# Kernel optimization log

Measured on AMD Instinct MI355X. Metric: run time of the kernel, lower is better.

## Reference

```python
import jax, jax.numpy as jnp
import numpy as np

DIM = 1024
NUM_HEADS = 16
HEAD_DIM = DIM // NUM_HEADS


def setup_inputs() -> dict:
    key = jax.random.key(0)
    k_x, k_q, k_k, k_v, k_o = jax.random.split(key, 5)
    B, L = 2, 2048
    scale = 1.0 / np.sqrt(DIM)
    x_bld = jax.random.normal(k_x, (B, L, DIM), dtype=jnp.float32)
    # LinearGeneral kernels: (in_features, num_heads, head_dim) for q/k/v,
    # (num_heads, head_dim, out_features) for out. Init ~ lecun_normal-ish scale.
    Wq = jax.random.normal(k_q, (DIM, NUM_HEADS, HEAD_DIM), dtype=jnp.float32) * scale
    Wk = jax.random.normal(k_k, (DIM, NUM_HEADS, HEAD_DIM), dtype=jnp.float32) * scale
    Wv = jax.random.normal(k_v, (DIM, NUM_HEADS, HEAD_DIM), dtype=jnp.float32) * scale
    Wo = jax.random.normal(k_o, (NUM_HEADS, HEAD_DIM, DIM), dtype=jnp.float32) * scale
    return {"x_bld": x_bld, "Wq": Wq, "Wk": Wk, "Wv": Wv, "Wo": Wo}


def reference(x_bld, Wq, Wk, Wv, Wo) -> jnp.ndarray:
    # Projections: [B,L,D] x [D,H,hd] -> [B,L,H,hd]
    q_blhd = jnp.einsum('bld,dhk->blhk', x_bld, Wq)
    k_blhd = jnp.einsum('bld,dhk->blhk', x_bld, Wk)
    v_blhd = jnp.einsum('bld,dhk->blhk', x_bld, Wv)
    # Scores: [B,H,L,L]
    attn_bhll = jnp.einsum('bqhd,bkhd->bhqk', q_blhd, k_blhd)
    attn_bhll = attn_bhll / jnp.sqrt(jnp.asarray(HEAD_DIM, dtype=attn_bhll.dtype))
    L = x_bld.shape[1]
    qi = jnp.arange(L)[:, None]
    ki = jnp.arange(L)[None, :]
    mask_ll = ki <= qi  # causal, no window
    neg_inf = jnp.finfo(attn_bhll.dtype).min
    attn_bhll = jnp.where(mask_ll[None, None, :, :], attn_bhll, neg_inf)
    attn_bhll = jax.nn.softmax(attn_bhll, axis=-1)
    y_blhd = jnp.einsum('bhqk,bkhd->bqhd', attn_bhll, v_blhd)
    # Output projection: contract (H, hd) -> D
    return jnp.einsum('blhk,hkd->bld', y_blhd, Wo)
```

## Files before the change

### kernel.cpp

```cpp
#include <hip/hip_runtime.h>
#include <hip/hip_bf16.h>

typedef __hip_bfloat16 bf16;
typedef __attribute__((ext_vector_type(8))) short short8;
typedef __attribute__((ext_vector_type(4))) float f32x4;

__device__ __forceinline__ float bfbits2f(unsigned short u) {
    return __uint_as_float(((unsigned int)u) << 16);
}
__device__ __forceinline__ unsigned short f2bfbits(float f) {
    union { float f; unsigned int u; } x;
    x.f = f;
    unsigned int r = x.u + 0x7FFFu + ((x.u >> 16) & 1u);
    return (unsigned short)(r >> 16);
}
__device__ __forceinline__ unsigned int pack_bf16x2(float lo, float hi) {
    unsigned int u0 = __float_as_uint(lo) + 0x8000u;
    unsigned int u1 = __float_as_uint(hi) + 0x8000u;
    return __builtin_amdgcn_perm(u1, u0, 0x07060302u);
}
__device__ __forceinline__ void async_copy16(const void* g, void* l) {
    __builtin_amdgcn_global_load_lds(
        (const __attribute__((address_space(1))) void*)g,
        (__attribute__((address_space(3))) void*)l, 16, 0, 0);
}

__global__ __launch_bounds__(256) void detect_dtype(
    const unsigned int* __restrict__ p0, const unsigned int* __restrict__ p1,
    const unsigned int* __restrict__ p2, const unsigned int* __restrict__ p3,
    const unsigned int* __restrict__ p4, int* __restrict__ flags) {
    const unsigned int* ps[5] = {p0, p1, p2, p3, p4};
    const unsigned int* p = ps[blockIdx.x];
    const int tid = threadIdx.x;
    int cnt = 0;
    for (int i = tid; i < 4096; i += 256) {
        unsigned int e = (p[i] >> 7) & 0xFFu;
        cnt += (e >= 90u && e <= 150u) ? 1 : 0;
    }
    __shared__ int r[256];
    r[tid] = cnt;
    __syncthreads();
    for (int off = 128; off; off >>= 1) {
        if (tid < off) r[tid] += r[tid + off];
        __syncthreads();
    }
    if (tid == 0) flags[blockIdx.x] = (r[0] > 2048) ? 1 : 0;
}

__global__ __launch_bounds__(256) void conv_x(const void* __restrict__ X,
                                              short* __restrict__ xb,
                                              const int* __restrict__ flags) {
    const bool isBf = flags[0] != 0;
    const int i = (blockIdx.x * 256 + threadIdx.x) * 8;
    if (isBf) {
        *(short8*)&xb[i] = *(const short8*)((const short*)X + i);
    } else {
        const float* xf = (const float*)X + i;
        float4 a = *(const float4*)xf;
        float4 b = *(const float4*)(xf + 4);
        short8 o;
        o[0] = (short)f2bfbits(a.x); o[1] = (short)f2bfbits(a.y);
        o[2] = (short)f2bfbits(a.z); o[3] = (short)f2bfbits(a.w);
        o[4] = (short)f2bfbits(b.x); o[5] = (short)f2bfbits(b.y);
        o[6] = (short)f2bfbits(b.z); o[7] = (short)f2bfbits(b.w);
        *(short8*)&xb[i] = o;
    }
}

__global__ __launch_bounds__(256) void conv_wT(
    const void* __restrict__ W1, const void* __restrict__ W2,
    const void* __restrict__ W3, const void* __restrict__ W4,
    short* __restrict__ O1, short* __restrict__ O2,
    short* __restrict__ O3, short* __restrict__ O4,
    const int* __restrict__ flags) {
    const void* Ws[4] = {W1, W2, W3, W4};
    short* Os[4] = {O1, O2, O3, O4};
    const int wsel = blockIdx.z;
    const bool isBf = flags[wsel + 1] != 0;
    const float scale = (wsel == 0) ? 0.125f : 1.0f;
    const void* W = Ws[wsel];
    short* O = Os[wsel];

    __shared__ float t[32][33];
    const int tx = threadIdx.x & 31;
    const int ty = threadIdx.x >> 5;
    const int gx = blockIdx.x * 32 + tx;
#pragma unroll
    for (int i = 0; i < 4; i++) {
        const int gy = blockIdx.y * 32 + ty + i * 8;
        float v = isBf ? bfbits2f(((const unsigned short*)W)[(size_t)gy * 1024 + gx])
                       : ((const float*)W)[(size_t)gy * 1024 + gx];
        t[ty + i * 8][tx] = v * scale;
    }
    __syncthreads();
#pragma unroll
    for (int i = 0; i < 4; i++) {
        const int orow = blockIdx.x * 32 + ty + i * 8;
        const int ocol = blockIdx.y * 32 + tx;
        O[(size_t)orow * 1024 + ocol] = (short)f2bfbits(t[tx][ty + i * 8]);
    }
}

__global__ __launch_bounds__(256) void transpose_v(const short* __restrict__ qkv,
                                                   short* __restrict__ VtG) {
    __shared__ short t[32][33];
    const int tx = threadIdx.x & 31, ty = threadIdx.x >> 5;
    const int b = blockIdx.z >> 4, h = blockIdx.z & 15;
    const int l0 = blockIdx.x * 32, d0 = blockIdx.y * 32;
#pragma unroll
    for (int i = 0; i < 4; i++) {
        const int l = l0 + ty + i * 8;
        t[ty + i * 8][tx] =
            qkv[(size_t)(b * 2048 + l) * 3072 + 2048 + h * 64 + d0 + tx];
    }
    __syncthreads();
    const int ptx = 2 * (tx & 15) + (tx >> 4);
#pragma unroll
    for (int i = 0; i < 4; i++) {
        const int d = d0 + ty + i * 8;
        VtG[((size_t)(b * 16 + h) * 64 + d) * 2048 + l0 + ptx] = t[tx][ty + i * 8];
    }
}

template <int BN>
__global__ __launch_bounds__(256) void gemm_async(const short* __restrict__ A,
                                                  const short* __restrict__ Bt,
                                                  void* __restrict__ C,
                                                  const int* __restrict__ flags,
                                                  int outIdx, int M, int N, int K) {
    __shared__ short As[2][128 * 32];
    __shared__ short Bs[2][BN * 32];
    constexpr int NI = BN / 32;

    const int tid = threadIdx.x;
    const int lane = tid & 63;
    const int wv = __builtin_amdgcn_readfirstlane(tid >> 6);
    const int quad = lane >> 4, l16 = lane & 15;
    const int wr = wv >> 1, wc = wv & 1;
    const int m0 = blockIdx.y * 128, n0 = blockIdx.x * BN;

    const int gr = lane >> 2;
    const int gc = (lane & 3) * 8;

    const f32x4 zero = {0.f, 0.f, 0.f, 0.f};
    f32x4 acc[4][NI];
#pragma unroll
    for (int mi = 0; mi < 4; mi++)
#pragma unroll
        for (int ni = 0; ni < NI; ni++) acc[mi][ni] = zero;

    const short* aptr[2];
    const short* bptr[BN / 64];
#pragma unroll
    for (int t = 0; t < 2; t++)
        aptr[t] = A + (size_t)(m0 + t * 64 + wv * 16 + gr) * K + gc;
#pragma unroll
    for (int t = 0; t < BN / 64; t++)
        bptr[t] = Bt + (size_t)(n0 + t * 64 + wv * 16 + gr) * K + gc;

#pragma unroll
    for (int t = 0; t < 2; t++) async_copy16(aptr[t], &As[0][(t * 64 + wv * 16) * 32]);
#pragma unroll
    for (int t = 0; t < BN / 64; t++) async_copy16(bptr[t], &Bs[0][(t * 64 + wv * 16) * 32]);

    for (int k0 = 0; k0 < K; k0 += 32) {
        const int cur = (k0 >> 5) & 1;
        __syncthreads();
        if (k0 + 32 < K) {
            const int nxt = cur ^ 1;
#pragma unroll
            for (int t = 0; t < 2; t++)
                async_copy16(aptr[t] + k0 + 32, &As[nxt][(t * 64 + wv * 16) * 32]);
#pragma unroll
            for (int t = 0; t < BN / 64; t++)
                async_copy16(bptr[t] + k0 + 32, &Bs[nxt][(t * 64 + wv * 16) * 32]);
        }

        short8 af[4], bfv[NI];
#pragma unroll
        for (int mi = 0; mi < 4; mi++)
            af[mi] = *(const short8*)&As[cur][(wr * 64 + mi * 16 + l16) * 32 + quad * 8];
#pragma unroll
        for (int ni = 0; ni < NI; ni++)
            bfv[ni] = *(const short8*)&Bs[cur][(wc * (BN / 2) + ni * 16 + l16) * 32 + quad * 8];
#pragma unroll
        for (int mi = 0; mi < 4; mi++)
#pragma unroll
            for (int ni = 0; ni < NI; ni++)
                acc[mi][ni] = __builtin_amdgcn_mfma_f32_16x16x32_bf16(
                    af[mi], bfv[ni], acc[mi][ni], 0, 0, 0);
    }

    const bool outBf = (outIdx < 0) ? true : (flags[outIdx] != 0);
    if (outBf) {
        unsigned short* Cb = (unsigned short*)C;
#pragma unroll
        for (int mi = 0; mi < 4; mi++)
#pragma unroll
            for (int ni = 0; ni < NI; ni++)
#pragma unroll
                for (int r = 0; r < 4; r++) {
                    const int row = m0 + wr * 64 + mi * 16 + quad * 4 + r;
                    const int col = n0 + wc * (BN / 2) + ni * 16 + l16;
                    Cb[(size_t)row * N + col] = f2bfbits(acc[mi][ni][r]);
                }
    } else {
        float* Cf = (float*)C;
#pragma unroll
        for (int mi = 0; mi < 4; mi++)
#pragma unroll
            for (int ni = 0; ni < NI; ni++)
#pragma unroll
                for (int r = 0; r < 4; r++) {
                    const int row = m0 + wr * 64 + mi * 16 + quad * 4 + r;
                    const int col = n0 + wc * (BN / 2) + ni * 16 + l16;
                    Cf[(size_t)row * N + col] = acc[mi][ni][r];
                }
    }
}

__global__ __launch_bounds__(256) void attn_mfma5(
    const short* __restrict__ qkv, const short* __restrict__ VtG,
    short* __restrict__ Yg, short* __restrict__ Opart, float* __restrict__ ml) {
    __shared__ short Ks[2][2 * 128 * 32];
    __shared__ short Vt[2][4 * 64 * 32];
    __shared__ short Ps[4 * 64 * 32];

    const int tid = threadIdx.x;
    const int lane = tid & 63;
    const int wv = __builtin_amdgcn_readfirstlane(tid >> 6);
    const int quad = lane >> 4, l16 = lane & 15;
    const int bh = blockIdx.x;
    const int b = bh >> 4, h = bh & 15;

    int qb, seg;
    const int slot = blockIdx.y;
    if (slot < 32) { qb = 31 - (slot >> 1); seg = slot & 1; }
    else { qb = 47 - slot; seg = -1; }

    const int ns = (qb + 2) >> 1;
    int sb0, sb1;
    if (seg < 0) { sb0 = 0; sb1 = ns; }
    else {
        const int half0 = ns >> 1;
        sb0 = seg ? half0 : 0;
        sb1 = seg ? ns : half0;
    }

    const int lr = lane >> 2;
    const int lc = (lane & 3) * 8;
    const short* kptr[4];
    const short* vptr[4];
    short* kdst[4];
    short* vdst[4];
#pragma unroll
    for (int i = 0; i < 4; i++) {
        const int u = wv * 4 + i;
        const int half = u & 1, kr0 = (u >> 1) * 16;
        kptr[i] = qkv + (size_t)(b * 2048 + sb0 * 128 + kr0 + lr) * 3072 + 1024 +
                  h * 64 + half * 32 + lc;
        kdst[i] = &Ks[0][(half * 128 + kr0) * 32];
        vptr[i] = VtG + ((size_t)bh * 64 + wv * 16 + lr) * 2048 + sb0 * 128 +
                  i * 32 + lc;
        vdst[i] = &Vt[0][(i * 64 + wv * 16) * 32];
    }
    const int kbufoff = (int)(&Ks[1][0] - &Ks[0][0]);
    const int vbufoff = (int)(&Vt[1][0] - &Vt[0][0]);
    const int buf0 = sb0 & 1;

#pragma unroll
    for (int i = 0; i < 2; i++) {
        const int qrow = qb * 64 + wv * 16 + lr;
        const short* src =
            qkv + (size_t)(b * 2048 + qrow) * 3072 + h * 64 + i * 32 + lc;
        async_copy16(src, &Ps[(i * 64 + wv * 16) * 32]);
    }
#pragma unroll
    for (int i = 0; i < 4; i++) {
        async_copy16(kptr[i], kdst[i] + buf0 * kbufoff);
        async_copy16(vptr[i], vdst[i] + buf0 * vbufoff);
        kptr[i] += 128 * 3072;
        vptr[i] += 128;
    }
    __syncthreads();
    const short8 qf0 = *(const short8*)&Ps[(wv * 16 + l16) * 32 + quad * 8];
    const short8 qf1 = *(const short8*)&Ps[(64 + wv * 16 + l16) * 32 + quad * 8];
    unsigned int* Psd = (unsigned int*)Ps;

    const f32x4 minit = {-12.f, -12.f, -12.f, -12.f};
    f32x4 O[4];
#pragma unroll
    for (int ni = 0; ni < 4; ni++) O[ni] = {0.f, 0.f, 0.f, 0.f};
    float l_st[4] = {0.f, 0.f, 0.f, 0.f};

    const int qrow0 = qb * 64 + wv * 16 + quad * 4;

    for (int sb = sb0; sb < sb1; sb++) {
        const int cur = sb & 1;
        if (sb != sb0) __syncthreads();
        if (sb + 1 < sb1) {
            const int nxt = cur ^ 1;
#pragma unroll
            for (int i = 0; i < 4; i++) {
                async_copy16(kptr[i], kdst[i] + nxt * kbufoff);
                async_copy16(vptr[i], vdst[i] + nxt * vbufoff);
                kptr[i] += 128 * 3072;
                vptr[i] += 128;
            }
        }
        const short* Kc = &Ks[0][0] + cur * kbufoff;
        const short* Vc = &Vt[0][0] + cur * vbufoff;

        f32x4 s[8];
#pragma unroll
        for (int ni = 0; ni < 8; ni++) {
            short8 kf0 = *(const short8*)&Kc[(ni * 16 + l16) * 32 + quad * 8];
            short8 kf1 = *(const short8*)&Kc[(128 + ni * 16 + l16) * 32 + quad * 8];
            s[ni] = __builtin_amdgcn_mfma_f32_16x16x32_bf16(qf0, kf0, minit, 0, 0, 0);
            s[ni] = __builtin_amdgcn_mfma_f32_16x16x32_bf16(qf1, kf1, s[ni], 0, 0, 0);
        }

        if (sb == ns - 1) {
#pragma unroll
            for (int ni = 0; ni < 8; ni++) {
                const int key = sb * 128 + ni * 16 + l16;
#pragma unroll
                for (int r = 0; r < 4; r++)
                    if (key > qrow0 + r) s[ni][r] = -1e30f;
            }
        }

#pragma unroll
        for (int ni = 0; ni < 8; ni++)
#pragma unroll
            for (int r = 0; r < 4; r++) s[ni][r] = __expf(s[ni][r]);
#pragma unroll
        for (int r = 0; r < 4; r++)
            l_st[r] += ((s[0][r] + s[1][r]) + (s[2][r] + s[3][r])) +
                       ((s[4][r] + s[5][r]) + (s[6][r] + s[7][r]));

#pragma unroll
        for (int c = 0; c < 4; c++)
#pragma unroll
            for (int r = 0; r < 4; r++)
                Psd[(c * 64 + wv * 16 + quad * 4 + r) * 16 + l16] =
                    pack_bf16x2(s[2 * c][r], s[2 * c + 1][r]);

        short8 pf[4];
#pragma unroll
        for (int c = 0; c < 4; c++)
            pf[c] = *(const short8*)&Ps[(c * 64 + wv * 16 + l16) * 32 + quad * 8];

#pragma unroll
        for (int ni = 0; ni < 4; ni++)
#pragma unroll
            for (int c = 0; c < 4; c++) {
                short8 vf = *(const short8*)&Vc[(c * 64 + ni * 16 + l16) * 32 + quad * 8];
                O[ni] = __builtin_amdgcn_mfma_f32_16x16x32_bf16(pf[c], vf, O[ni], 0, 0, 0);
            }
    }

    float lt[4];
#pragma unroll
    for (int r = 0; r < 4; r++) {
        float v = l_st[r];
        v += __shfl_xor(v, 1);
        v += __shfl_xor(v, 2);
        v += __shfl_xor(v, 4);
        v += __shfl_xor(v, 8);
        lt[r] = v;
    }

    if (seg < 0) {
#pragma unroll
        for (int r = 0; r < 4; r++) {
            const float inv = 1.f / lt[r];
            const int qrow = qrow0 + r;
#pragma unroll
            for (int ni = 0; ni < 4; ni++)
                Yg[(size_t)(b * 2048 + qrow) * 1024 + h * 64 + ni * 16 + l16] =
                    (short)f2bfbits(O[ni][r] * inv);
        }
    } else {
        const int qb16 = qb - 16;
        const int base = ((seg * 32 + bh) * 16 + qb16) * 64;
#pragma unroll
        for (int r = 0; r < 4; r++) {
            const int q = wv * 16 + quad * 4 + r;
#pragma unroll
            for (int ni = 0; ni < 4; ni++)
                Opart[(size_t)(base + q) * 64 + ni * 16 + l16] =
                    (short)f2bfbits(O[ni][r]);
            if (l16 == 0) ml[base + q] = lt[r];
        }
    }
}

__global__ __launch_bounds__(256) void attn_combine(
    const short* __restrict__ Opart, const float* __restrict__ ml,
    short* __restrict__ Yg) {
    const int qb16 = blockIdx.x;
    const int bh = blockIdx.y;
    const int b = bh >> 4, h = bh & 15;
    const int tid = threadIdx.x;
    const int q = tid >> 2;
    const int d0 = (tid & 3) * 16;

    const int i0 = ((0 * 32 + bh) * 16 + qb16) * 64 + q;
    const int i1 = ((1 * 32 + bh) * 16 + qb16) * 64 + q;
    const float inv = 1.f / (ml[i0] + ml[i1]);

    const short* p0 = Opart + (size_t)i0 * 64 + d0;
    const short* p1 = Opart + (size_t)i1 * 64 + d0;
    short8 x0 = *(const short8*)p0, y0 = *(const short8*)p1;
    short8 x1 = *(const short8*)(p0 + 8), y1 = *(const short8*)(p1 + 8);
    short8 o0, o1;
#pragma unroll
    for (int t = 0; t < 8; t++) {
        o0[t] = (short)f2bfbits((bfbits2f((unsigned short)x0[t]) +
                                 bfbits2f((unsigned short)y0[t])) * inv);
        o1[t] = (short)f2bfbits((bfbits2f((unsigned short)x1[t]) +
                                 bfbits2f((unsigned short)y1[t])) * inv);
    }
    const int qrow = (16 + qb16) * 64 + q;
    short* yp = Yg + (size_t)(b * 2048 + qrow) * 1024 + h * 64 + d0;
    *(short8*)yp = o0;
    *(short8*)(yp + 8) = o1;
}

extern "C" void kernel_launch(void* const* d_in, const int* in_sizes, int n_in,
                              void* d_out, int out_size, void* d_ws, size_t ws_size,
                              hipStream_t stream) {
    const int M = 2 * 2048;
    const int D = 1024;

    char* w = (char*)d_ws;
    int* flags = (int*)w;
    short* xb  = (short*)(w + 4096);
    short* WqT = (short*)(w + 4096 + (8u << 20));
    short* WkT = WqT + (1u << 20);
    short* WvT = WkT + (1u << 20);
    short* WoT = WvT + (1u << 20);
    short* qkv = WoT + (1u << 20);
    short* VtG = qkv + (size_t)M * 3072;
    short* Opart = VtG + (size_t)2048 * 2048;
    float* mlp = (float*)(Opart + (size_t)2 * 32 * 16 * 64 * 64);
    short* y = xb;

    detect_dtype<<<5, 256, 0, stream>>>(
        (const unsigned int*)d_in[0], (const unsigned int*)d_in[1],
        (const unsigned int*)d_in[2], (const unsigned int*)d_in[3],
        (const unsigned int*)d_in[4], flags);

    conv_x<<<2048, 256, 0, stream>>>(d_in[0], xb, flags);
    conv_wT<<<dim3(32, 32, 4), 256, 0, stream>>>(
        d_in[1], d_in[2], d_in[3], d_in[4], WqT, WkT, WvT, WoT, flags);

    gemm_async<128><<<dim3(3072 / 128, M / 128), 256, 0, stream>>>(
        xb, WqT, qkv, flags, -1, M, 3072, D);

    transpose_v<<<dim3(64, 2, 32), 256, 0, stream>>>(qkv, VtG);

    attn_mfma5<<<dim3(32, 48), 256, 0, stream>>>(qkv, VtG, y, Opart, mlp);
    attn_combine<<<dim3(16, 32), 256, 0, stream>>>(Opart, mlp, y);

    gemm_async<64><<<dim3(D / 64, M / 128), 256, 0, stream>>>(
        y, WoT, d_out, flags, 0, M, D, D);
}
```

Measured before the change: 196.2 us.

## Shrink attention key tiles to 64, split work 4/2/1 ways, fuse prep kernels

The attention kernel now uses 64-key tiles instead of 128 and splits each query block's key range into 4, 2 or 1 segments depending on causal length. This balances work across more blocks (88 slots per head instead of 48) and uses less LDS per block, and the combine kernel is generalized to merge a variable number of partials. The dtype-detection, x conversion and weight transpose kernels are merged into one prep kernel that checks the dtype inside each wavefront with a ballot, which removes two launches and the flags buffer. In exchange there are more partial outputs to write and merge, and the dtype check is repeated in every block and in the output GEMM.

```diff
diff --git a/kernel.cpp b/kernel.cpp
--- a/kernel.cpp
+++ b/kernel.cpp
@@ -24,80 +24,68 @@
         (const __attribute__((address_space(1))) void*)g,
         (__attribute__((address_space(3))) void*)l, 16, 0, 0);
 }
-
-__global__ __launch_bounds__(256) void detect_dtype(
-    const unsigned int* __restrict__ p0, const unsigned int* __restrict__ p1,
-    const unsigned int* __restrict__ p2, const unsigned int* __restrict__ p3,
-    const unsigned int* __restrict__ p4, int* __restrict__ flags) {
-    const unsigned int* ps[5] = {p0, p1, p2, p3, p4};
-    const unsigned int* p = ps[blockIdx.x];
+__device__ __forceinline__ bool sniff_bf16(const unsigned int* p, int lane) {
+    unsigned int wd = p[lane];
+    unsigned int e = (wd >> 7) & 0xFFu;
+    return __popcll(__ballot(e >= 90u && e <= 150u)) > 40;
+}
+
+__global__ __launch_bounds__(256) void prep(
+    const void* __restrict__ X, const void* __restrict__ W1,
+    const void* __restrict__ W2, const void* __restrict__ W3,
+    const void* __restrict__ W4, short* __restrict__ xb,
+    short* __restrict__ O1, short* __restrict__ O2,
+    short* __restrict__ O3, short* __restrict__ O4) {
+    __shared__ float tbuf[32][33];
+    const int bx = blockIdx.x;
     const int tid = threadIdx.x;
-    int cnt = 0;
-    for (int i = tid; i < 4096; i += 256) {
-        unsigned int e = (p[i] >> 7) & 0xFFu;
-        cnt += (e >= 90u && e <= 150u) ? 1 : 0;
-    }
-    __shared__ int r[256];
-    r[tid] = cnt;
-    __syncthreads();
-    for (int off = 128; off; off >>= 1) {
-        if (tid < off) r[tid] += r[tid + off];
+    const int lane = tid & 63;
+
+    if (bx < 2048) {
+        const bool isBf = sniff_bf16((const unsigned int*)X, lane);
+        const int i = (bx * 256 + tid) * 8;
+        if (isBf) {
+            *(short8*)&xb[i] = *(const short8*)((const short*)X + i);
+        } else {
+            const float* xf = (const float*)X + i;
+            float4 a = *(const float4*)xf;
+            float4 b = *(const float4*)(xf + 4);
+            short8 o;
+            o[0] = (short)f2bfbits(a.x); o[1] = (short)f2bfbits(a.y);
+            o[2] = (short)f2bfbits(a.z); o[3] = (short)f2bfbits(a.w);
+            o[4] = (short)f2bfbits(b.x); o[5] = (short)f2bfbits(b.y);
+            o[6] = (short)f2bfbits(b.z); o[7] = (short)f2bfbits(b.w);
+            *(short8*)&xb[i] = o;
+        }
+    } else {
+        const void* Ws[4] = {W1, W2, W3, W4};
+        short* Os[4] = {O1, O2, O3, O4};
+        const int t = bx - 2048;
+        const int wsel = t >> 10;
+        const int tile = t & 1023;
+        const int bxt = tile & 31, byt = tile >> 5;
+        const void* W = Ws[wsel];
+        const bool isBf = sniff_bf16((const unsigned int*)W, lane);
+        const float scale = (wsel == 0) ? 0.125f : 1.0f;
+        short* O = Os[wsel];
+
+        const int tx = tid & 31, ty = tid >> 5;
+        const int gx = bxt * 32 + tx;
+#pragma unroll
+        for (int i = 0; i < 4; i++) {
+            const int gy = byt * 32 + ty + i * 8;
+            float v = isBf
+                ? bfbits2f(((const unsigned short*)W)[(size_t)gy * 1024 + gx])
+                : ((const float*)W)[(size_t)gy * 1024 + gx];
+            tbuf[ty + i * 8][tx] = v * scale;
+        }
         __syncthreads();
-    }
-    if (tid == 0) flags[blockIdx.x] = (r[0] > 2048) ? 1 : 0;
-}
-
-__global__ __launch_bounds__(256) void conv_x(const void* __restrict__ X,
-                                              short* __restrict__ xb,
-                                              const int* __restrict__ flags) {
-    const bool isBf = flags[0] != 0;
-    const int i = (blockIdx.x * 256 + threadIdx.x) * 8;
-    if (isBf) {
-        *(short8*)&xb[i] = *(const short8*)((const short*)X + i);
-    } else {
-        const float* xf = (const float*)X + i;
-        float4 a = *(const float4*)xf;
-        float4 b = *(const float4*)(xf + 4);
-        short8 o;
-        o[0] = (short)f2bfbits(a.x); o[1] = (short)f2bfbits(a.y);
-        o[2] = (short)f2bfbits(a.z); o[3] = (short)f2bfbits(a.w);
-        o[4] = (short)f2bfbits(b.x); o[5] = (short)f2bfbits(b.y);
-        o[6] = (short)f2bfbits(b.z); o[7] = (short)f2bfbits(b.w);
-        *(short8*)&xb[i] = o;
-    }
-}
-
-__global__ __launch_bounds__(256) void conv_wT(
-    const void* __restrict__ W1, const void* __restrict__ W2,
-    const void* __restrict__ W3, const void* __restrict__ W4,
-    short* __restrict__ O1, short* __restrict__ O2,
-    short* __restrict__ O3, short* __restrict__ O4,
-    const int* __restrict__ flags) {
-    const void* Ws[4] = {W1, W2, W3, W4};
-    short* Os[4] = {O1, O2, O3, O4};
-    const int wsel = blockIdx.z;
-    const bool isBf = flags[wsel + 1] != 0;
-    const float scale = (wsel == 0) ? 0.125f : 1.0f;
-    const void* W = Ws[wsel];
-    short* O = Os[wsel];
-
-    __shared__ float t[32][33];
-    const int tx = threadIdx.x & 31;
-    const int ty = threadIdx.x >> 5;
-    const int gx = blockIdx.x * 32 + tx;
-#pragma unroll
-    for (int i = 0; i < 4; i++) {
-        const int gy = blockIdx.y * 32 + ty + i * 8;
-        float v = isBf ? bfbits2f(((const unsigned short*)W)[(size_t)gy * 1024 + gx])
-                       : ((const float*)W)[(size_t)gy * 1024 + gx];
-        t[ty + i * 8][tx] = v * scale;
-    }
-    __syncthreads();
-#pragma unroll
-    for (int i = 0; i < 4; i++) {
-        const int orow = blockIdx.x * 32 + ty + i * 8;
-        const int ocol = blockIdx.y * 32 + tx;
-        O[(size_t)orow * 1024 + ocol] = (short)f2bfbits(t[tx][ty + i * 8]);
+#pragma unroll
+        for (int i = 0; i < 4; i++) {
+            const int orow = bxt * 32 + ty + i * 8;
+            const int ocol = byt * 32 + tx;
+            O[(size_t)orow * 1024 + ocol] = (short)f2bfbits(tbuf[tx][ty + i * 8]);
+        }
     }
 }
 
@@ -126,8 +114,8 @@
 __global__ __launch_bounds__(256) void gemm_async(const short* __restrict__ A,
                                                   const short* __restrict__ Bt,
                                                   void* __restrict__ C,
-                                                  const int* __restrict__ flags,
-                                                  int outIdx, int M, int N, int K) {
+                                                  const unsigned int* __restrict__ xdet,
+                                                  int M, int N, int K) {
     __shared__ short As[2][128 * 32];
     __shared__ short Bs[2][BN * 32];
     constexpr int NI = BN / 32;
@@ -191,7 +179,8 @@
                     af[mi], bfv[ni], acc[mi][ni], 0, 0, 0);
     }
 
-    const bool outBf = (outIdx < 0) ? true : (flags[outIdx] != 0);
+    bool outBf = true;
+    if (xdet) outBf = sniff_bf16(xdet, lane);
     if (outBf) {
         unsigned short* Cb = (unsigned short*)C;
 #pragma unroll
@@ -219,12 +208,12 @@
     }
 }
 
-__global__ __launch_bounds__(256) void attn_mfma5(
+__global__ __launch_bounds__(256) void attn_mfma6(
     const short* __restrict__ qkv, const short* __restrict__ VtG,
     short* __restrict__ Yg, short* __restrict__ Opart, float* __restrict__ ml) {
-    __shared__ short Ks[2][2 * 128 * 32];
-    __shared__ short Vt[2][4 * 64 * 32];
-    __shared__ short Ps[4 * 64 * 32];
+    __shared__ short Ks[2][2 * 64 * 32];
+    __shared__ short Vt[2][2 * 64 * 32];
+    __shared__ short Ps[2 * 64 * 32];
 
     const int tid = threadIdx.x;
     const int lane = tid & 63;
@@ -233,66 +222,61 @@
     const int bh = blockIdx.x;
     const int b = bh >> 4, h = bh & 15;
 
-    int qb, seg;
+    int qb, seg, S;
     const int slot = blockIdx.y;
-    if (slot < 32) { qb = 31 - (slot >> 1); seg = slot & 1; }
-    else { qb = 47 - slot; seg = -1; }
-
-    const int ns = (qb + 2) >> 1;
-    int sb0, sb1;
-    if (seg < 0) { sb0 = 0; sb1 = ns; }
-    else {
-        const int half0 = ns >> 1;
-        sb0 = seg ? half0 : 0;
-        sb1 = seg ? ns : half0;
-    }
+    if (slot < 64)      { qb = 31 - (slot >> 2); seg = slot & 3; S = 4; }
+    else if (slot < 80) { const int t2 = slot - 64; qb = 15 - (t2 >> 1); seg = t2 & 1; S = 2; }
+    else                { qb = 87 - slot; seg = 0; S = 1; }
+
+    const int ns = qb + 1;
+    const int sb0 = seg * ns / S;
+    const int sb1 = (seg + 1) * ns / S;
 
     const int lr = lane >> 2;
     const int lc = (lane & 3) * 8;
-    const short* kptr[4];
-    const short* vptr[4];
-    short* kdst[4];
-    short* vdst[4];
-#pragma unroll
-    for (int i = 0; i < 4; i++) {
-        const int u = wv * 4 + i;
-        const int half = u & 1, kr0 = (u >> 1) * 16;
-        kptr[i] = qkv + (size_t)(b * 2048 + sb0 * 128 + kr0 + lr) * 3072 + 1024 +
+
+    const short* kptr[2];
+    const short* vptr[2];
+    short* kdst[2];
+    short* vdst[2];
+#pragma unroll
+    for (int i = 0; i < 2; i++) {
+        const int u = wv * 2 + i;
+        const int half = u & 1, g16 = (u >> 1) * 16;
+        kptr[i] = qkv + (size_t)(b * 2048 + sb0 * 64 + g16 + lr) * 3072 + 1024 +
                   h * 64 + half * 32 + lc;
-        kdst[i] = &Ks[0][(half * 128 + kr0) * 32];
-        vptr[i] = VtG + ((size_t)bh * 64 + wv * 16 + lr) * 2048 + sb0 * 128 +
-                  i * 32 + lc;
-        vdst[i] = &Vt[0][(i * 64 + wv * 16) * 32];
-    }
-    const int kbufoff = (int)(&Ks[1][0] - &Ks[0][0]);
-    const int vbufoff = (int)(&Vt[1][0] - &Vt[0][0]);
+        kdst[i] = &Ks[0][(half * 64 + g16) * 32];
+        vptr[i] = VtG + ((size_t)bh * 64 + g16 + lr) * 2048 + sb0 * 64 +
+                  half * 32 + lc;
+        vdst[i] = &Vt[0][(half * 64 + g16) * 32];
+    }
+    const int bufoff = 2 * 64 * 32;
     const int buf0 = sb0 & 1;
+    const int qbuf = buf0 ^ 1;
 
 #pragma unroll
     for (int i = 0; i < 2; i++) {
-        const int qrow = qb * 64 + wv * 16 + lr;
-        const short* src =
-            qkv + (size_t)(b * 2048 + qrow) * 3072 + h * 64 + i * 32 + lc;
-        async_copy16(src, &Ps[(i * 64 + wv * 16) * 32]);
-    }
-#pragma unroll
-    for (int i = 0; i < 4; i++) {
-        async_copy16(kptr[i], kdst[i] + buf0 * kbufoff);
-        async_copy16(vptr[i], vdst[i] + buf0 * vbufoff);
-        kptr[i] += 128 * 3072;
-        vptr[i] += 128;
+        const int u = wv * 2 + i;
+        const int half = u & 1, g16 = (u >> 1) * 16;
+        const short* qsrc = qkv + (size_t)(b * 2048 + qb * 64 + g16 + lr) * 3072 +
+                            h * 64 + half * 32 + lc;
+        async_copy16(qsrc, &Ks[qbuf][(half * 64 + g16) * 32]);
+        async_copy16(kptr[i], kdst[i] + buf0 * bufoff);
+        async_copy16(vptr[i], vdst[i] + buf0 * bufoff);
+        kptr[i] += 64 * 3072;
+        vptr[i] += 64;
     }
     __syncthreads();
-    const short8 qf0 = *(const short8*)&Ps[(wv * 16 + l16) * 32 + quad * 8];
-    const short8 qf1 = *(const short8*)&Ps[(64 + wv * 16 + l16) * 32 + quad * 8];
+    const short8 qf0 = *(const short8*)&Ks[qbuf][(wv * 16 + l16) * 32 + quad * 8];
+    const short8 qf1 = *(const short8*)&Ks[qbuf][(64 + wv * 16 + l16) * 32 + quad * 8];
+    __syncthreads();
+
     unsigned int* Psd = (unsigned int*)Ps;
-
     const f32x4 minit = {-12.f, -12.f, -12.f, -12.f};
     f32x4 O[4];
 #pragma unroll
     for (int ni = 0; ni < 4; ni++) O[ni] = {0.f, 0.f, 0.f, 0.f};
     float l_st[4] = {0.f, 0.f, 0.f, 0.f};
-
     const int qrow0 = qb * 64 + wv * 16 + quad * 4;
 
     for (int sb = sb0; sb < sb1; sb++) {
@@ -301,29 +285,29 @@
         if (sb + 1 < sb1) {
             const int nxt = cur ^ 1;
 #pragma unroll
-            for (int i = 0; i < 4; i++) {
-                async_copy16(kptr[i], kdst[i] + nxt * kbufoff);
-                async_copy16(vptr[i], vdst[i] + nxt * vbufoff);
-                kptr[i] += 128 * 3072;
-                vptr[i] += 128;
+            for (int i = 0; i < 2; i++) {
+                async_copy16(kptr[i], kdst[i] + nxt * bufoff);
+                async_copy16(vptr[i], vdst[i] + nxt * bufoff);
+                kptr[i] += 64 * 3072;
+                vptr[i] += 64;
             }
         }
-        const short* Kc = &Ks[0][0] + cur * kbufoff;
-        const short* Vc = &Vt[0][0] + cur * vbufoff;
-
-        f32x4 s[8];
-#pragma unroll
-        for (int ni = 0; ni < 8; ni++) {
+        const short* Kc = &Ks[cur][0];
+        const short* Vc = &Vt[cur][0];
+
+        f32x4 s[4];
+#pragma unroll
+        for (int ni = 0; ni < 4; ni++) {
             short8 kf0 = *(const short8*)&Kc[(ni * 16 + l16) * 32 + quad * 8];
-            short8 kf1 = *(const short8*)&Kc[(128 + ni * 16 + l16) * 32 + quad * 8];
+            short8 kf1 = *(const short8*)&Kc[(64 + ni * 16 + l16) * 32 + quad * 8];
             s[ni] = __builtin_amdgcn_mfma_f32_16x16x32_bf16(qf0, kf0, minit, 0, 0, 0);
             s[ni] = __builtin_amdgcn_mfma_f32_16x16x32_bf16(qf1, kf1, s[ni], 0, 0, 0);
         }
 
-        if (sb == ns - 1) {
-#pragma unroll
-            for (int ni = 0; ni < 8; ni++) {
-                const int key = sb * 128 + ni * 16 + l16;
+        if (sb == qb) {
+#pragma unroll
+            for (int ni = 0; ni < 4; ni++) {
+                const int key = sb * 64 + ni * 16 + l16;
 #pragma unroll
                 for (int r = 0; r < 4; r++)
                     if (key > qrow0 + r) s[ni][r] = -1e30f;
@@ -331,30 +315,29 @@
         }
 
 #pragma unroll
-        for (int ni = 0; ni < 8; ni++)
+        for (int ni = 0; ni < 4; ni++)
 #pragma unroll
             for (int r = 0; r < 4; r++) s[ni][r] = __expf(s[ni][r]);
 #pragma unroll
         for (int r = 0; r < 4; r++)
-            l_st[r] += ((s[0][r] + s[1][r]) + (s[2][r] + s[3][r])) +
-                       ((s[4][r] + s[5][r]) + (s[6][r] + s[7][r]));
-
-#pragma unroll
-        for (int c = 0; c < 4; c++)
+            l_st[r] += (s[0][r] + s[1][r]) + (s[2][r] + s[3][r]);
+
+#pragma unroll
+        for (int c = 0; c < 2; c++)
 #pragma unroll
             for (int r = 0; r < 4; r++)
                 Psd[(c * 64 + wv * 16 + quad * 4 + r) * 16 + l16] =
                     pack_bf16x2(s[2 * c][r], s[2 * c + 1][r]);
 
-        short8 pf[4];
-#pragma unroll
-        for (int c = 0; c < 4; c++)
+        short8 pf[2];
+#pragma unroll
+        for (int c = 0; c < 2; c++)
             pf[c] = *(const short8*)&Ps[(c * 64 + wv * 16 + l16) * 32 + quad * 8];
 
 #pragma unroll
         for (int ni = 0; ni < 4; ni++)
 #pragma unroll
-            for (int c = 0; c < 4; c++) {
+            for (int c = 0; c < 2; c++) {
                 short8 vf = *(const short8*)&Vc[(c * 64 + ni * 16 + l16) * 32 + quad * 8];
                 O[ni] = __builtin_amdgcn_mfma_f32_16x16x32_bf16(pf[c], vf, O[ni], 0, 0, 0);
             }
@@ -371,7 +354,7 @@
         lt[r] = v;
     }
 
-    if (seg < 0) {
+    if (S == 1) {
 #pragma unroll
         for (int r = 0; r < 4; r++) {
             const float inv = 1.f / lt[r];
@@ -382,8 +365,8 @@
                     (short)f2bfbits(O[ni][r] * inv);
         }
     } else {
-        const int qb16 = qb - 16;
-        const int base = ((seg * 32 + bh) * 16 + qb16) * 64;
+        const int qidx = qb - 8;
+        const int base = ((seg * 32 + bh) * 24 + qidx) * 64;
 #pragma unroll
         for (int r = 0; r < 4; r++) {
             const int q = wv * 16 + quad * 4 + r;
@@ -396,34 +379,40 @@
     }
 }
 
-__global__ __launch_bounds__(256) void attn_combine(
+__global__ __launch_bounds__(256) void attn_combine6(
     const short* __restrict__ Opart, const float* __restrict__ ml,
     short* __restrict__ Yg) {
-    const int qb16 = blockIdx.x;
+    const int qb = 8 + blockIdx.x;
     const int bh = blockIdx.y;
     const int b = bh >> 4, h = bh & 15;
+    const int S = (qb >= 16) ? 4 : 2;
+    const int qidx = qb - 8;
     const int tid = threadIdx.x;
     const int q = tid >> 2;
     const int d0 = (tid & 3) * 16;
 
-    const int i0 = ((0 * 32 + bh) * 16 + qb16) * 64 + q;
-    const int i1 = ((1 * 32 + bh) * 16 + qb16) * 64 + q;
-    const float inv = 1.f / (ml[i0] + ml[i1]);
-
-    const short* p0 = Opart + (size_t)i0 * 64 + d0;
-    const short* p1 = Opart + (size_t)i1 * 64 + d0;
-    short8 x0 = *(const short8*)p0, y0 = *(const short8*)p1;
-    short8 x1 = *(const short8*)(p0 + 8), y1 = *(const short8*)(p1 + 8);
+    float a0[8] = {}, a1[8] = {};
+    float lsum = 0.f;
+    for (int s = 0; s < S; s++) {
+        const int idx = ((s * 32 + bh) * 24 + qidx) * 64 + q;
+        lsum += ml[idx];
+        const short* p = Opart + (size_t)idx * 64 + d0;
+        short8 x0 = *(const short8*)p;
+        short8 x1 = *(const short8*)(p + 8);
+#pragma unroll
+        for (int t = 0; t < 8; t++) {
+            a0[t] += bfbits2f((unsigned short)x0[t]);
+            a1[t] += bfbits2f((unsigned short)x1[t]);
+        }
+    }
+    const float inv = 1.f / lsum;
     short8 o0, o1;
 #pragma unroll
     for (int t = 0; t < 8; t++) {
-        o0[t] = (short)f2bfbits((bfbits2f((unsigned short)x0[t]) +
-                                 bfbits2f((unsigned short)y0[t])) * inv);
-        o1[t] = (short)f2bfbits((bfbits2f((unsigned short)x1[t]) +
-                                 bfbits2f((unsigned short)y1[t])) * inv);
-    }
-    const int qrow = (16 + qb16) * 64 + q;
-    short* yp = Yg + (size_t)(b * 2048 + qrow) * 1024 + h * 64 + d0;
+        o0[t] = (short)f2bfbits(a0[t] * inv);
+        o1[t] = (short)f2bfbits(a1[t] * inv);
+    }
+    short* yp = Yg + (size_t)(b * 2048 + qb * 64 + q) * 1024 + h * 64 + d0;
     *(short8*)yp = o0;
     *(short8*)(yp + 8) = o1;
 }
@@ -435,35 +424,28 @@
     const int D = 1024;
 
     char* w = (char*)d_ws;
-    int* flags = (int*)w;
-    short* xb  = (short*)(w + 4096);
-    short* WqT = (short*)(w + 4096 + (8u << 20));
+    short* xb  = (short*)w;
+    short* WqT = (short*)(w + (8u << 20));
     short* WkT = WqT + (1u << 20);
     short* WvT = WkT + (1u << 20);
     short* WoT = WvT + (1u << 20);
     short* qkv = WoT + (1u << 20);
     short* VtG = qkv + (size_t)M * 3072;
     short* Opart = VtG + (size_t)2048 * 2048;
-    float* mlp = (float*)(Opart + (size_t)2 * 32 * 16 * 64 * 64);
+    float* mlp = (float*)(Opart + (size_t)4 * 32 * 24 * 64 * 64);
     short* y = xb;
 
-    detect_dtype<<<5, 256, 0, stream>>>(
-        (const unsigned int*)d_in[0], (const unsigned int*)d_in[1],
-        (const unsigned int*)d_in[2], (const unsigned int*)d_in[3],
-        (const unsigned int*)d_in[4], flags);
-
-    conv_x<<<2048, 256, 0, stream>>>(d_in[0], xb, flags);
-    conv_wT<<<dim3(32, 32, 4), 256, 0, stream>>>(
-        d_in[1], d_in[2], d_in[3], d_in[4], WqT, WkT, WvT, WoT, flags);
+    prep<<<6144, 256, 0, stream>>>(d_in[0], d_in[1], d_in[2], d_in[3], d_in[4],
+                                   xb, WqT, WkT, WvT, WoT);
 
     gemm_async<128><<<dim3(3072 / 128, M / 128), 256, 0, stream>>>(
-        xb, WqT, qkv, flags, -1, M, 3072, D);
+        xb, WqT, qkv, nullptr, M, 3072, D);
 
     transpose_v<<<dim3(64, 2, 32), 256, 0, stream>>>(qkv, VtG);
 
-    attn_mfma5<<<dim3(32, 48), 256, 0, stream>>>(qkv, VtG, y, Opart, mlp);
-    attn_combine<<<dim3(16, 32), 256, 0, stream>>>(Opart, mlp, y);
+    attn_mfma6<<<dim3(32, 88), 256, 0, stream>>>(qkv, VtG, y, Opart, mlp);
+    attn_combine6<<<dim3(24, 32), 256, 0, stream>>>(Opart, mlp, y);
 
     gemm_async<64><<<dim3(D / 64, M / 128), 256, 0, stream>>>(
-        y, WoT, d_out, flags, 0, M, D, D);
-}
+        y, WoT, d_out, (const unsigned int*)d_in[0], M, D, D);
+}
```

Result: faster. 189.2 us (-3.5%).
